# Performance work log

Measured on AMD Instinct MI355X. Metric: run time of the kernel, lower is better.

Reference implementation:

```python
import jax, jax.numpy as jnp
import numpy as np


def setup_inputs() -> dict:
    key = jax.random.key(0)
    ks = jax.random.split(key, 3)
    B, H, W, C = 32, 56, 56, 512
    N = H * W
    x = jax.random.normal(ks[0], (B, N, C), dtype=jnp.float32)
    # learned params (qkv_bias=False)
    w_qkv = jax.random.normal(ks[1], (C, 3 * C), dtype=jnp.float32) * (C ** -0.5)
    w_proj = jax.random.normal(ks[2], (C, C), dtype=jnp.float32) * (C ** -0.5)
    b_proj = jnp.zeros((C,), dtype=jnp.float32)
    return {"x": x, "w_qkv": w_qkv, "w_proj": w_proj, "b_proj": b_proj,
            "H": H, "W": W}


def reference(x, w_qkv, w_proj, b_proj, H, W):
    num_heads, ws = 8, 7
    B, N, C = x.shape
    hd = C // num_heads
    scale = hd ** -0.5
    hg, wg = H // ws, W // ws
    G = hg * wg  # total groups
    S = ws * ws  # tokens per window
    # window partition: [B,N,C] -> [B,G,S,C]
    xw = x.reshape(B, hg, ws, wg, ws, C).transpose(0, 1, 3, 2, 4, 5)
    xw = xw.reshape(B, G, S, C)
    # qkv projection -> [3,B,G,heads,S,hd]
    qkv = (xw @ w_qkv).reshape(B, G, S, 3, num_heads, hd)
    qkv = qkv.transpose(3, 0, 1, 4, 2, 5)
    q, k, v = qkv[0], qkv[1], qkv[2]
    attn = jnp.einsum('bghqd,bghkd->bghqk', q, k) * scale
    attn = jax.nn.softmax(attn, axis=-1)
    out = jnp.einsum('bghqk,bghkd->bghqd', attn, v)
    # merge heads: [B,G,h,S,d] -> [B,G,S,C]
    out = out.transpose(0, 1, 3, 2, 4).reshape(B, G, S, C)
    # window merge: [B,G,S,C] -> [B,N,C]
    out = out.reshape(B, hg, wg, ws, ws, C).transpose(0, 1, 3, 2, 4, 5)
    out = out.reshape(B, N, C)
    return out @ w_proj + b_proj
```

## Files before the change

### kernel.cpp

```cpp
#include <hip/hip_runtime.h>

typedef unsigned short ushort;
typedef unsigned int uint;
typedef __bf16 bf16x8 __attribute__((ext_vector_type(8)));
typedef unsigned short u16x8 __attribute__((ext_vector_type(8)));
typedef float f32x4 __attribute__((ext_vector_type(4)));

__device__ __forceinline__ ushort f2bf(float f) {
  uint u = __builtin_bit_cast(uint, f);
  u += 0x7fffu + ((u >> 16) & 1u);
  return (ushort)(u >> 16);
}

__device__ __forceinline__ f32x4 mfma_bf16(u16x8 a, u16x8 b, f32x4 c) {
  return __builtin_amdgcn_mfma_f32_16x16x32_bf16(
      __builtin_bit_cast(bf16x8, a), __builtin_bit_cast(bf16x8, b), c, 0, 0, 0);
}

__global__ void cvt_transpose(const float* __restrict__ W, ushort* __restrict__ WT,
                              int N, int total) {
  int idx = blockIdx.x * 256 + threadIdx.x;
  if (idx >= total) return;
  int n = idx >> 9, k = idx & 511;
  WT[idx] = f2bf(W[(size_t)k * N + n]);
}

__global__ __launch_bounds__(256) void gemm_qkv(const float* __restrict__ X,
                                                const ushort* __restrict__ BT,
                                                ushort* __restrict__ C) {
  __shared__ __align__(16) ushort as_[128 * 32];
  __shared__ __align__(16) ushort bs_[128 * 32];
  const int tid = threadIdx.x;
  const int lane = tid & 63;
  const int wid = tid >> 6;
  const int c16 = lane & 15, q4 = lane >> 4;
  const int m0 = blockIdx.x * 128;
  const int n0 = blockIdx.y * 128;
  const int wr = (wid >> 1) * 64, wc = (wid & 1) * 64;

  f32x4 acc[4][4];
#pragma unroll
  for (int m = 0; m < 4; ++m)
#pragma unroll
    for (int n = 0; n < 4; ++n) acc[m][n] = f32x4{0.f, 0.f, 0.f, 0.f};

  const float* aptr = X + (size_t)(m0 + (tid >> 1)) * 512 + (tid & 1) * 16;
  const ushort* bptr = BT + (size_t)(n0 + (tid >> 2)) * 512 + (tid & 3) * 8;
  ushort* awr = as_ + (tid >> 1) * 32 + (tid & 1) * 16;
  auto bl0 = (__attribute__((address_space(3))) uint*)(bs_ + tid * 8);
  auto bl1 = (__attribute__((address_space(3))) uint*)(bs_ + 2048 + tid * 8);

  const ushort* ard = as_ + (wr + c16) * 32 + q4 * 8;
  const ushort* brd = bs_ + (wc + c16) * 32 + q4 * 8;

  for (int k0 = 0; k0 < 512; k0 += 32) {
    if (k0) __syncthreads();
    __builtin_amdgcn_global_load_lds(
        (__attribute__((address_space(1))) uint*)(bptr + k0), bl0, 16, 0, 0);
    __builtin_amdgcn_global_load_lds(
        (__attribute__((address_space(1))) uint*)(bptr + 64 * 512 + k0), bl1, 16, 0, 0);
    f32x4 a0 = *(const f32x4*)(aptr + k0);
    f32x4 a1 = *(const f32x4*)(aptr + k0 + 4);
    f32x4 a2 = *(const f32x4*)(aptr + k0 + 8);
    f32x4 a3 = *(const f32x4*)(aptr + k0 + 12);
    u16x8 p0, p1;
#pragma unroll
    for (int j = 0; j < 4; ++j) {
      p0[j] = f2bf(a0[j]); p0[j + 4] = f2bf(a1[j]);
      p1[j] = f2bf(a2[j]); p1[j + 4] = f2bf(a3[j]);
    }
    *reinterpret_cast<u16x8*>(awr) = p0;
    *reinterpret_cast<u16x8*>(awr + 8) = p1;
    __syncthreads();
    u16x8 af[4], bf[4];
#pragma unroll
    for (int m = 0; m < 4; ++m) af[m] = *reinterpret_cast<const u16x8*>(ard + m * 512);
#pragma unroll
    for (int n = 0; n < 4; ++n) bf[n] = *reinterpret_cast<const u16x8*>(brd + n * 512);
#pragma unroll
    for (int m = 0; m < 4; ++m)
#pragma unroll
      for (int n = 0; n < 4; ++n) acc[m][n] = mfma_bf16(af[m], bf[n], acc[m][n]);
  }
  const int row0 = m0 + wr + q4 * 4;
  const int col0 = n0 + wc + c16;
#pragma unroll
  for (int m = 0; m < 4; ++m)
#pragma unroll
    for (int r = 0; r < 4; ++r) {
      ushort* cp = C + (size_t)(row0 + m * 16 + r) * 1536 + col0;
      cp[0]  = f2bf(acc[m][0][r]);
      cp[16] = f2bf(acc[m][1][r]);
      cp[32] = f2bf(acc[m][2][r]);
      cp[48] = f2bf(acc[m][3][r]);
    }
}

__global__ __launch_bounds__(256) void attn_win(const ushort* __restrict__ qkv,
                                                ushort* __restrict__ O) {
  __shared__ __align__(16) ushort p_lds[4][4096];
  __shared__ __align__(16) ushort v_lds[4][4096];
  const int tid = threadIdx.x, lane = tid & 63, w = tid >> 6;
  const int wg = blockIdx.x * 4 + w;
  const int head = wg & 7, g = (wg >> 3) & 63, b = wg >> 9;
  const int gh = g >> 3, gw = g & 7;
  const int c16 = lane & 15, q4 = lane >> 4;
  const size_t brow = (size_t)b * 3136;
  const u16x8 Z = {0, 0, 0, 0, 0, 0, 0, 0};

  int rowq[4]; bool val[4];
#pragma unroll
  for (int i = 0; i < 4; ++i) {
    int s = i * 16 + c16;
    val[i] = (s < 49);
    int ss = val[i] ? s : 0;
    rowq[i] = (gh * 7 + ss / 7) * 56 + gw * 7 + ss % 7;
  }
  const int qc = head * 64 + q4 * 8;

  u16x8 qf[2][4], kf[2][4];
#pragma unroll
  for (int i = 0; i < 4; ++i) {
    const ushort* p = qkv + (brow + rowq[i]) * 1536 + qc;
#pragma unroll
    for (int kk = 0; kk < 2; ++kk) {
      qf[kk][i] = val[i] ? *reinterpret_cast<const u16x8*>(p + kk * 32) : Z;
      kf[kk][i] = val[i] ? *reinterpret_cast<const u16x8*>(p + 512 + kk * 32) : Z;
    }
  }

  {
    int t = lane < 49 ? lane : 0;
    const ushort* vp =
        qkv + (brow + ((gh * 7 + t / 7) * 56 + gw * 7 + t % 7)) * 1536 + 1024 + head * 64;
    u16x8 vr[8];
#pragma unroll
    for (int j = 0; j < 8; ++j)
      vr[j] = (lane < 49) ? *reinterpret_cast<const u16x8*>(vp + j * 8) : Z;
#pragma unroll
    for (int d = 0; d < 64; ++d)
      v_lds[w][(d * 64 + lane) ^ ((d & 7) << 3)] = vr[d >> 3][d & 7];
  }

  f32x4 acc[4][4];
#pragma unroll
  for (int m = 0; m < 4; ++m)
#pragma unroll
    for (int n = 0; n < 4; ++n) acc[m][n] = f32x4{0.f, 0.f, 0.f, 0.f};
#pragma unroll
  for (int kk = 0; kk < 2; ++kk)
#pragma unroll
    for (int m = 0; m < 4; ++m)
#pragma unroll
      for (int n = 0; n < 4; ++n)
        acc[m][n] = mfma_bf16(qf[kk][m], kf[kk][n], acc[m][n]);

#pragma unroll
  for (int m = 0; m < 4; ++m)
#pragma unroll
    for (int r = 0; r < 4; ++r) {
      float s0 = acc[m][0][r] * 0.125f;
      float s1 = acc[m][1][r] * 0.125f;
      float s2 = acc[m][2][r] * 0.125f;
      float s3 = (c16 == 0) ? acc[m][3][r] * 0.125f : -1e30f;
      float mx = fmaxf(fmaxf(s0, s1), fmaxf(s2, s3));
#pragma unroll
      for (int off = 1; off < 16; off <<= 1) mx = fmaxf(mx, __shfl_xor(mx, off));
      s0 = __expf(s0 - mx);
      s1 = __expf(s1 - mx);
      s2 = __expf(s2 - mx);
      s3 = (c16 == 0) ? __expf(s3 - mx) : 0.f;
      float sum = s0 + s1 + s2 + s3;
#pragma unroll
      for (int off = 1; off < 16; off <<= 1) sum += __shfl_xor(sum, off);
      float inv = 1.f / sum;
      int row = m * 16 + q4 * 4 + r;
      int rb = row * 64, sw = (row & 7) << 3;
      p_lds[w][(rb + c16) ^ sw]      = f2bf(s0 * inv);
      p_lds[w][(rb + 16 + c16) ^ sw] = f2bf(s1 * inv);
      p_lds[w][(rb + 32 + c16) ^ sw] = f2bf(s2 * inv);
      p_lds[w][(rb + 48 + c16) ^ sw] = f2bf(s3 * inv);
    }
  __syncthreads();

  f32x4 o[4][4];
#pragma unroll
  for (int m = 0; m < 4; ++m)
#pragma unroll
    for (int n = 0; n < 4; ++n) o[m][n] = f32x4{0.f, 0.f, 0.f, 0.f};
#pragma unroll
  for (int kk = 0; kk < 2; ++kk) {
    u16x8 pa[4], vb[4];
#pragma unroll
    for (int m = 0; m < 4; ++m) {
      int row = m * 16 + c16;
      pa[m] = *reinterpret_cast<const u16x8*>(
          &p_lds[w][(row * 64 + kk * 32 + q4 * 8) ^ ((row & 7) << 3)]);
    }
#pragma unroll
    for (int n = 0; n < 4; ++n) {
      int d = n * 16 + c16;
      vb[n] = *reinterpret_cast<const u16x8*>(
          &v_lds[w][(d * 64 + kk * 32 + q4 * 8) ^ ((d & 7) << 3)]);
    }
#pragma unroll
    for (int m = 0; m < 4; ++m)
#pragma unroll
      for (int n = 0; n < 4; ++n) o[m][n] = mfma_bf16(pa[m], vb[n], o[m][n]);
  }

#pragma unroll
  for (int m = 0; m < 4; ++m)
#pragma unroll
    for (int r = 0; r < 4; ++r) {
      int s = m * 16 + q4 * 4 + r;
      if (s < 49) {
        int n_tok = (gh * 7 + s / 7) * 56 + gw * 7 + s % 7;
        ushort* op = O + (brow + n_tok) * 512 + head * 64 + c16;
        op[0]  = f2bf(o[m][0][r]);
        op[16] = f2bf(o[m][1][r]);
        op[32] = f2bf(o[m][2][r]);
        op[48] = f2bf(o[m][3][r]);
      }
    }
}

__global__ __launch_bounds__(256) void gemm_proj(const ushort* __restrict__ A,
                                                 const ushort* __restrict__ BT,
                                                 const float* __restrict__ bias,
                                                 float* __restrict__ C) {
  __shared__ __align__(16) ushort as_[128 * 32];
  __shared__ __align__(16) ushort bs_[128 * 32];
  const int tid = threadIdx.x;
  const int lane = tid & 63;
  const int wid = tid >> 6;
  const int c16 = lane & 15, q4 = lane >> 4;
  const int m0 = blockIdx.x * 128, n0 = blockIdx.y * 128;
  const int wr = (wid >> 1) * 64, wc = (wid & 1) * 64;

  f32x4 acc[4][4];
#pragma unroll
  for (int m = 0; m < 4; ++m)
#pragma unroll
    for (int n = 0; n < 4; ++n) acc[m][n] = f32x4{0.f, 0.f, 0.f, 0.f};

  const ushort* aptr = A + (size_t)(m0 + (tid >> 2)) * 512 + (tid & 3) * 8;
  const ushort* bptr = BT + (size_t)(n0 + (tid >> 2)) * 512 + (tid & 3) * 8;
  auto al0 = (__attribute__((address_space(3))) uint*)(as_ + tid * 8);
  auto al1 = (__attribute__((address_space(3))) uint*)(as_ + 2048 + tid * 8);
  auto bl0 = (__attribute__((address_space(3))) uint*)(bs_ + tid * 8);
  auto bl1 = (__attribute__((address_space(3))) uint*)(bs_ + 2048 + tid * 8);
  const ushort* ard = as_ + (wr + c16) * 32 + q4 * 8;
  const ushort* brd = bs_ + (wc + c16) * 32 + q4 * 8;

  for (int k0 = 0; k0 < 512; k0 += 32) {
    if (k0) __syncthreads();
    __builtin_amdgcn_global_load_lds(
        (__attribute__((address_space(1))) uint*)(aptr + k0), al0, 16, 0, 0);
    __builtin_amdgcn_global_load_lds(
        (__attribute__((address_space(1))) uint*)(aptr + 64 * 512 + k0), al1, 16, 0, 0);
    __builtin_amdgcn_global_load_lds(
        (__attribute__((address_space(1))) uint*)(bptr + k0), bl0, 16, 0, 0);
    __builtin_amdgcn_global_load_lds(
        (__attribute__((address_space(1))) uint*)(bptr + 64 * 512 + k0), bl1, 16, 0, 0);
    __syncthreads();
    u16x8 af[4], bf[4];
#pragma unroll
    for (int m = 0; m < 4; ++m) af[m] = *reinterpret_cast<const u16x8*>(ard + m * 512);
#pragma unroll
    for (int n = 0; n < 4; ++n) bf[n] = *reinterpret_cast<const u16x8*>(brd + n * 512);
#pragma unroll
    for (int m = 0; m < 4; ++m)
#pragma unroll
      for (int n = 0; n < 4; ++n) acc[m][n] = mfma_bf16(af[m], bf[n], acc[m][n]);
  }
  const int row0 = m0 + wr + q4 * 4;
  const int col0 = n0 + wc + c16;
  const float b0 = bias[col0], b1 = bias[col0 + 16], b2 = bias[col0 + 32], b3 = bias[col0 + 48];
#pragma unroll
  for (int m = 0; m < 4; ++m)
#pragma unroll
    for (int r = 0; r < 4; ++r) {
      float* cp = C + (size_t)(row0 + m * 16 + r) * 512 + col0;
      cp[0]  = acc[m][0][r] + b0;
      cp[16] = acc[m][1][r] + b1;
      cp[32] = acc[m][2][r] + b2;
      cp[48] = acc[m][3][r] + b3;
    }
}

extern "C" void kernel_launch(void* const* d_in, const int* in_sizes, int n_in,
                              void* d_out, int out_size, void* d_ws, size_t ws_size,
                              hipStream_t stream) {
  const float* x      = (const float*)d_in[0];
  const float* w_qkv  = (const float*)d_in[1];
  const float* w_proj = (const float*)d_in[2];
  const float* b_proj = (const float*)d_in[3];
  char* ws = (char*)d_ws;
  ushort* wqkvT  = (ushort*)ws;
  ushort* wprojT = (ushort*)(ws + 1572864);
  ushort* qkv    = (ushort*)(ws + 2097152);
  ushort* attn   = (ushort*)(ws + 310378496);
  float* out = (float*)d_out;

  cvt_transpose<<<3072, 256, 0, stream>>>(w_qkv, wqkvT, 1536, 1536 * 512);
  cvt_transpose<<<1024, 256, 0, stream>>>(w_proj, wprojT, 512, 512 * 512);
  gemm_qkv<<<dim3(784, 12), 256, 0, stream>>>(x, wqkvT, qkv);
  attn_win<<<4096, 256, 0, stream>>>(qkv, attn);
  gemm_proj<<<dim3(784, 4), 256, 0, stream>>>(attn, wprojT, b_proj, out);
}
```

Before: 607.4 us.

## Pre-convert X to bf16 and load both GEMM operands via direct-to-LDS loads

Adds a standalone pass that converts the fp32 input X to bf16 once, so the QKV GEMM no longer re-reads fp32 X and converts it in every one of its 12 column-block passes. Both A and B tiles are now loaded with global_load_lds. The weight conversion becomes a shared-memory tiled transpose with coalesced reads, and the bf16 X buffer is reused for the attention output. The cost is an extra kernel plus an extra write and read of the activation tensor.

Result: faster. 520.7 us (-14.3%).

```diff
diff --git a/kernel.cpp b/kernel.cpp
--- a/kernel.cpp
+++ b/kernel.cpp
@@ -17,25 +17,48 @@
       __builtin_bit_cast(bf16x8, a), __builtin_bit_cast(bf16x8, b), c, 0, 0, 0);
 }
 
-__global__ void cvt_transpose(const float* __restrict__ W, ushort* __restrict__ WT,
-                              int N, int total) {
-  int idx = blockIdx.x * 256 + threadIdx.x;
-  if (idx >= total) return;
-  int n = idx >> 9, k = idx & 511;
-  WT[idx] = f2bf(W[(size_t)k * N + n]);
-}
-
-__global__ __launch_bounds__(256) void gemm_qkv(const float* __restrict__ X,
-                                                const ushort* __restrict__ BT,
-                                                ushort* __restrict__ C) {
+__global__ __launch_bounds__(256) void cvt_x(const float* __restrict__ X,
+                                             ushort* __restrict__ Xb, int total8) {
+  int stride = gridDim.x * 256;
+  for (int i = blockIdx.x * 256 + threadIdx.x; i < total8; i += stride) {
+    f32x4 a = ((const f32x4*)X)[2 * i];
+    f32x4 b = ((const f32x4*)X)[2 * i + 1];
+    u16x8 o;
+#pragma unroll
+    for (int j = 0; j < 4; ++j) { o[j] = f2bf(a[j]); o[j + 4] = f2bf(b[j]); }
+    ((u16x8*)Xb)[i] = o;
+  }
+}
+
+__global__ __launch_bounds__(256) void transpose_cvt(const float* __restrict__ W,
+                                                     ushort* __restrict__ WT,
+                                                     int K, int N) {
+  __shared__ float t[32][33];
+  const int tn0 = blockIdx.x * 32, tk0 = blockIdx.y * 32;
+  const int tx = threadIdx.x & 31, ty = threadIdx.x >> 5;
+#pragma unroll
+  for (int i = 0; i < 4; ++i) {
+    int k = tk0 + ty + i * 8;
+    t[ty + i * 8][tx] = W[(size_t)k * N + tn0 + tx];
+  }
+  __syncthreads();
+#pragma unroll
+  for (int i = 0; i < 4; ++i) {
+    int n = tn0 + ty + i * 8;
+    WT[(size_t)n * K + tk0 + tx] = f2bf(t[tx][ty + i * 8]);
+  }
+}
+
+__global__ __launch_bounds__(256) void gemm_qkv2(const ushort* __restrict__ A,
+                                                 const ushort* __restrict__ BT,
+                                                 ushort* __restrict__ C) {
   __shared__ __align__(16) ushort as_[128 * 32];
   __shared__ __align__(16) ushort bs_[128 * 32];
   const int tid = threadIdx.x;
   const int lane = tid & 63;
   const int wid = tid >> 6;
   const int c16 = lane & 15, q4 = lane >> 4;
-  const int m0 = blockIdx.x * 128;
-  const int n0 = blockIdx.y * 128;
+  const int m0 = blockIdx.x * 128, n0 = blockIdx.y * 128;
   const int wr = (wid >> 1) * 64, wc = (wid & 1) * 64;
 
   f32x4 acc[4][4];
@@ -44,33 +67,25 @@
 #pragma unroll
     for (int n = 0; n < 4; ++n) acc[m][n] = f32x4{0.f, 0.f, 0.f, 0.f};
 
-  const float* aptr = X + (size_t)(m0 + (tid >> 1)) * 512 + (tid & 1) * 16;
+  const ushort* aptr = A + (size_t)(m0 + (tid >> 2)) * 512 + (tid & 3) * 8;
   const ushort* bptr = BT + (size_t)(n0 + (tid >> 2)) * 512 + (tid & 3) * 8;
-  ushort* awr = as_ + (tid >> 1) * 32 + (tid & 1) * 16;
+  auto al0 = (__attribute__((address_space(3))) uint*)(as_ + tid * 8);
+  auto al1 = (__attribute__((address_space(3))) uint*)(as_ + 2048 + tid * 8);
   auto bl0 = (__attribute__((address_space(3))) uint*)(bs_ + tid * 8);
   auto bl1 = (__attribute__((address_space(3))) uint*)(bs_ + 2048 + tid * 8);
-
   const ushort* ard = as_ + (wr + c16) * 32 + q4 * 8;
   const ushort* brd = bs_ + (wc + c16) * 32 + q4 * 8;
 
   for (int k0 = 0; k0 < 512; k0 += 32) {
     if (k0) __syncthreads();
     __builtin_amdgcn_global_load_lds(
+        (__attribute__((address_space(1))) uint*)(aptr + k0), al0, 16, 0, 0);
+    __builtin_amdgcn_global_load_lds(
+        (__attribute__((address_space(1))) uint*)(aptr + 64 * 512 + k0), al1, 16, 0, 0);
+    __builtin_amdgcn_global_load_lds(
         (__attribute__((address_space(1))) uint*)(bptr + k0), bl0, 16, 0, 0);
     __builtin_amdgcn_global_load_lds(
         (__attribute__((address_space(1))) uint*)(bptr + 64 * 512 + k0), bl1, 16, 0, 0);
-    f32x4 a0 = *(const f32x4*)(aptr + k0);
-    f32x4 a1 = *(const f32x4*)(aptr + k0 + 4);
-    f32x4 a2 = *(const f32x4*)(aptr + k0 + 8);
-    f32x4 a3 = *(const f32x4*)(aptr + k0 + 12);
-    u16x8 p0, p1;
-#pragma unroll
-    for (int j = 0; j < 4; ++j) {
-      p0[j] = f2bf(a0[j]); p0[j + 4] = f2bf(a1[j]);
-      p1[j] = f2bf(a2[j]); p1[j + 4] = f2bf(a3[j]);
-    }
-    *reinterpret_cast<u16x8*>(awr) = p0;
-    *reinterpret_cast<u16x8*>(awr + 8) = p1;
     __syncthreads();
     u16x8 af[4], bf[4];
 #pragma unroll
@@ -299,13 +314,14 @@
   char* ws = (char*)d_ws;
   ushort* wqkvT  = (ushort*)ws;
   ushort* wprojT = (ushort*)(ws + 1572864);
-  ushort* qkv    = (ushort*)(ws + 2097152);
-  ushort* attn   = (ushort*)(ws + 310378496);
+  ushort* xb     = (ushort*)(ws + 2097152);
+  ushort* qkv    = (ushort*)(ws + 104857600);
   float* out = (float*)d_out;
 
-  cvt_transpose<<<3072, 256, 0, stream>>>(w_qkv, wqkvT, 1536, 1536 * 512);
-  cvt_transpose<<<1024, 256, 0, stream>>>(w_proj, wprojT, 512, 512 * 512);
-  gemm_qkv<<<dim3(784, 12), 256, 0, stream>>>(x, wqkvT, qkv);
-  attn_win<<<4096, 256, 0, stream>>>(qkv, attn);
-  gemm_proj<<<dim3(784, 4), 256, 0, stream>>>(attn, wprojT, b_proj, out);
-}
+  transpose_cvt<<<dim3(48, 16), 256, 0, stream>>>(w_qkv, wqkvT, 512, 1536);
+  transpose_cvt<<<dim3(16, 16), 256, 0, stream>>>(w_proj, wprojT, 512, 512);
+  cvt_x<<<2048, 256, 0, stream>>>(x, xb, 100352 * 512 / 8);
+  gemm_qkv2<<<dim3(784, 12), 256, 0, stream>>>(xb, wqkvT, qkv);
+  attn_win<<<4096, 256, 0, stream>>>(qkv, xb);
+  gemm_proj<<<dim3(784, 4), 256, 0, stream>>>(xb, wprojT, b_proj, out);
+}
```
